# Kernel optimization log

Measured on AMD Instinct MI355X. Metric: run time of the kernel, lower is better.

The kernel has to match this reference:

```python
import jax, jax.numpy as jnp
import numpy as np

EPS = 1e-8  # torch F.cosine_similarity default eps


def setup_inputs() -> dict:
    key = jax.random.key(0)
    k1, k2 = jax.random.split(key)
    x = jax.random.normal(k1, (16384, 1024), dtype=jnp.float32)
    label = jax.random.randint(k2, (16384, 64), 0, 2).astype(jnp.int64)
    w = jnp.asarray(10.0, dtype=jnp.float32)  # nn.Parameter init_w
    b = jnp.asarray(-5.0, dtype=jnp.float32)  # nn.Parameter init_b
    return {"x": x, "label": label, "w": w, "b": b}


def reference(x, label, w, b):
    # Append the 'no-label' column for rows whose label vector is all zero.
    extra = (label.sum(axis=1) == 0).astype(label.dtype)[:, None]
    lab = jnp.concatenate([label, extra], axis=1).astype(x.dtype)  # [B, C]

    counts = lab.sum(axis=0)                  # [C] positives per centroid
    active = counts > 0                       # torch drops empty columns; we mask them

    # Centroids: mean of x over rows carrying each label (scatter-mean as GEMM).
    anchor = (lab.T @ x) / jnp.maximum(counts, 1.0)[:, None]   # [C, D]

    # Cosine similarity between every sample and every centroid.
    xn = jnp.maximum(jnp.linalg.norm(x, axis=1), EPS)          # [B]
    an = jnp.maximum(jnp.linalg.norm(anchor, axis=1), EPS)     # [C]
    cos = (x @ anchor.T) / (xn[:, None] * an[None, :])          # [B, C]

    logits = cos * w + b
    # Removing empty columns from softmax == setting their logits to -inf.
    logits = jnp.where(active[None, :], logits, -jnp.inf)
    logp = jax.nn.log_softmax(logits, axis=1)                   # [B, C]

    # Row expansion in torch duplicates sample i once per positive label j;
    # the logits row only depends on i, so CE over expanded rows is a
    # pair-weighted mean of -logp[i, j] over positive (i, j) pairs.
    n_pairs = lab.sum()
    nloss = -jnp.sum(jnp.where(lab > 0, logp, 0.0)) / n_pairs
    return nloss
```

## Files before the change

### kernel.cpp

```cpp
#include <hip/hip_runtime.h>
#include <hip/hip_bf16.h>
#include <stdint.h>

#define NROWS 16384
#define NDIM  1024
#define NLAB  64
#define NC    65
#define CPAD  80

typedef float float4v __attribute__((ext_vector_type(4)));
typedef short short8  __attribute__((ext_vector_type(8)));

static constexpr size_t SCALE_B = 0;
static constexpr size_t ACTB_B  = 320;
static constexpr size_t WSUM_B  = 400;
static constexpr size_t CNTF_B  = 448;
static constexpr size_t CNTP_B  = 1024;
static constexpr size_t MASK_B  = 83968;
static constexpr size_t XN2_B   = 215040;
static constexpr size_t LFRAG_B = 280576;
static constexpr size_t BFRAG_B = 2902016;
static constexpr size_t XAF_B   = 3065856;
static constexpr size_t PART_B  = 70174720;
static constexpr size_t SLAB    = (size_t)CPAD * NDIM * 4;
static constexpr size_t ANCH_SZ = (size_t)CPAD * NDIM * 4;
static constexpr size_t NRM_SZ  = (size_t)CPAD * 4 * 4;

__device__ __forceinline__ unsigned short bf16u(float f) {
    __hip_bfloat16 h = __float2bfloat16(f);
    return __builtin_bit_cast(unsigned short, h);
}
__device__ __forceinline__ unsigned pk2(float a, float b) {
    return (unsigned)bf16u(a) | ((unsigned)bf16u(b) << 16);
}

__global__ __launch_bounds__(256, 4) void k01_prep(const float* __restrict__ x,
                                                   const int* __restrict__ label,
                                                   unsigned short* __restrict__ xAfrag,
                                                   float* __restrict__ xn2g,
                                                   unsigned long long* __restrict__ masks,
                                                   unsigned* __restrict__ cntpart,
                                                   unsigned short* __restrict__ lfrag) {
    __shared__ unsigned cnt[NC];
    __shared__ unsigned long long smask[64];
    __shared__ float red[4][16];
    int t = threadIdx.x;
    if (blockIdx.x < 1024) {
        int rt = blockIdx.x;
        int w = t >> 6, lane = t & 63, q = lane >> 4, col = lane & 15;
        const float* rowp = x + ((size_t)rt * 16 + col) * NDIM;
        uint4* dst = (uint4*)xAfrag + ((size_t)rt * 32 + w * 8) * 64 + lane;
        float sq = 0.f;
#pragma unroll
        for (int kb = 0; kb < 8; ++kb) {
            int d0 = w * 256 + kb * 32 + q * 8;
            float4 fa = *(const float4*)(rowp + d0);
            float4 fb = *(const float4*)(rowp + d0 + 4);
            sq += fa.x * fa.x + fa.y * fa.y + fa.z * fa.z + fa.w * fa.w
                + fb.x * fb.x + fb.y * fb.y + fb.z * fb.z + fb.w * fb.w;
            uint4 v;
            v.x = pk2(fa.x, fa.y); v.y = pk2(fa.z, fa.w);
            v.z = pk2(fb.x, fb.y); v.w = pk2(fb.z, fb.w);
            dst[kb * 64] = v;
        }
        sq += __shfl_xor(sq, 16, 64);
        sq += __shfl_xor(sq, 32, 64);
        if (q == 0) red[w][col] = sq;
        __syncthreads();
        if (t < 16) xn2g[rt * 16 + t] = red[0][t] + red[1][t] + red[2][t] + red[3][t];
        return;
    }
    int bid = blockIdx.x - 1024;
    if (t < NC) cnt[t] = 0;
    __syncthreads();
    int wave = t >> 6, lane = t & 63;
    int rowblock = bid * 64;
    unsigned creg = 0, zreg = 0;
#pragma unroll 4
    for (int p = 0; p < 16; ++p) {
        int row = rowblock + p * 4 + wave;
        int v = label[row * NLAB + lane];
        unsigned long long m = __ballot(v != 0);
        creg += (unsigned)((m >> lane) & 1ull);
        if (lane == 0) {
            masks[row] = m;
            smask[p * 4 + wave] = m;
            zreg += (m == 0ull) ? 1u : 0u;
        }
    }
    atomicAdd(&cnt[lane], creg);
    if (lane == 0 && zreg) atomicAdd(&cnt[64], zreg);
    __syncthreads();
    if (t < 80) cntpart[bid * 80 + t] = (t < NC) ? cnt[t] : 0u;
    for (int pid = t; pid < 640; pid += 256) {
        int rt2l = pid / 320, rem = pid % 320;
        int ct = rem >> 6, ln = rem & 63;
        int q = ln >> 4, col = ln & 15;
        int c = ct * 16 + col;
        int rbase = rt2l * 32 + q * 8;
        unsigned pk[4];
#pragma unroll
        for (int jp = 0; jp < 4; ++jp) {
            unsigned long long m0 = smask[rbase + jp * 2], m1 = smask[rbase + jp * 2 + 1];
            unsigned b0, b1;
            if (c < 64)       { b0 = (unsigned)((m0 >> c) & 1ull); b1 = (unsigned)((m1 >> c) & 1ull); }
            else if (c == 64) { b0 = (m0 == 0ull); b1 = (m1 == 0ull); }
            else              { b0 = 0u; b1 = 0u; }
            pk[jp] = (b0 ? 0x3F80u : 0u) | (b1 ? 0x3F800000u : 0u);
        }
        uint4 w = make_uint4(pk[0], pk[1], pk[2], pk[3]);
        ((uint4*)lfrag)[((size_t)(bid * 2 + rt2l) * 5 + ct) * 64 + ln] = w;
    }
}

__global__ __launch_bounds__(256) void k2_sums(const float* __restrict__ x,
                                               const unsigned short* __restrict__ lfrag,
                                               float* __restrict__ partial,
                                               int kslices) {
    int t = threadIdx.x, wave = t >> 6, lane = t & 63;
    int q = lane >> 4, col = lane & 15;
    int dgroup = blockIdx.x & 15, ks = blockIdx.x >> 4;
    int nkb = (NROWS / kslices) >> 5;
    int kb0 = ks * nkb;
    int d = dgroup * 64 + wave * 16 + col;
    const uint4* A = (const uint4*)lfrag;
    const float* xb = x + d;

    float4v acc[5];
#pragma unroll
    for (int ct = 0; ct < 5; ++ct) acc[ct] = (float4v){0.f, 0.f, 0.f, 0.f};

    float f0[8], f1[8];
    uint4 a0[5], a1[5];
    {
        const float* p = xb + (size_t)(kb0 * 32 + q * 8) * NDIM;
#pragma unroll
        for (int j = 0; j < 8; ++j) f0[j] = p[(size_t)j * NDIM];
#pragma unroll
        for (int ct = 0; ct < 5; ++ct) a0[ct] = A[((size_t)kb0 * 5 + ct) * 64 + lane];
        const float* p1 = xb + (size_t)((kb0 + 1) * 32 + q * 8) * NDIM;
#pragma unroll
        for (int j = 0; j < 8; ++j) f1[j] = p1[(size_t)j * NDIM];
#pragma unroll
        for (int ct = 0; ct < 5; ++ct) a1[ct] = A[((size_t)(kb0 + 1) * 5 + ct) * 64 + lane];
    }

    for (int i = 0; i < nkb; i += 2) {
        int p2 = i + 2 < nkb ? kb0 + i + 2 : kb0 + i;
        int p3 = i + 3 < nkb ? kb0 + i + 3 : kb0 + i + 1;
        {
            uint4 bq;
            bq.x = pk2(f0[0], f0[1]); bq.y = pk2(f0[2], f0[3]);
            bq.z = pk2(f0[4], f0[5]); bq.w = pk2(f0[6], f0[7]);
            short8 bf = __builtin_bit_cast(short8, bq);
#pragma unroll
            for (int ct = 0; ct < 5; ++ct) {
                short8 af = __builtin_bit_cast(short8, a0[ct]);
                acc[ct] = __builtin_amdgcn_mfma_f32_16x16x32_bf16(af, bf, acc[ct], 0, 0, 0);
            }
            const float* p = xb + (size_t)(p2 * 32 + q * 8) * NDIM;
#pragma unroll
            for (int j = 0; j < 8; ++j) f0[j] = p[(size_t)j * NDIM];
#pragma unroll
            for (int ct = 0; ct < 5; ++ct) a0[ct] = A[((size_t)p2 * 5 + ct) * 64 + lane];
        }
        {
            uint4 bq;
            bq.x = pk2(f1[0], f1[1]); bq.y = pk2(f1[2], f1[3]);
            bq.z = pk2(f1[4], f1[5]); bq.w = pk2(f1[6], f1[7]);
            short8 bf = __builtin_bit_cast(short8, bq);
#pragma unroll
            for (int ct = 0; ct < 5; ++ct) {
                short8 af = __builtin_bit_cast(short8, a1[ct]);
                acc[ct] = __builtin_amdgcn_mfma_f32_16x16x32_bf16(af, bf, acc[ct], 0, 0, 0);
            }
            const float* p = xb + (size_t)(p3 * 32 + q * 8) * NDIM;
#pragma unroll
            for (int j = 0; j < 8; ++j) f1[j] = p[(size_t)j * NDIM];
#pragma unroll
            for (int ct = 0; ct < 5; ++ct) a1[ct] = A[((size_t)p3 * 5 + ct) * 64 + lane];
        }
    }
    float* pb = partial + (size_t)ks * CPAD * NDIM;
#pragma unroll
    for (int ct = 0; ct < 5; ++ct)
#pragma unroll
        for (int reg = 0; reg < 4; ++reg)
            pb[(size_t)(ct * 16 + q * 4 + reg) * NDIM + d] = acc[ct][reg];
}

__global__ __launch_bounds__(256) void k2bA(const float* __restrict__ partial,
                                            int kslices,
                                            float* __restrict__ anchor_raw,
                                            float* __restrict__ norm2part) {
    __shared__ float red[4];
    int c = blockIdx.x >> 2, dq = blockIdx.x & 3, t = threadIdx.x;
    int d = dq * 256 + t;
    const float* p = partial + (size_t)c * NDIM + d;
    float s = 0.f;
#pragma unroll 8
    for (int sl = 0; sl < kslices; ++sl) s += p[(size_t)sl * CPAD * NDIM];
    anchor_raw[(size_t)c * NDIM + d] = s;
    float ss = s * s;
#pragma unroll
    for (int m = 32; m >= 1; m >>= 1) ss += __shfl_xor(ss, m, 64);
    if ((t & 63) == 0) red[t >> 6] = ss;
    __syncthreads();
    if (t == 0) norm2part[blockIdx.x] = red[0] + red[1] + red[2] + red[3];
}

__global__ __launch_bounds__(1024) void k2bB(const float* __restrict__ wptr,
                                             const unsigned* __restrict__ cntpart,
                                             const float* __restrict__ anchor_raw,
                                             const float* __restrict__ norm2part,
                                             unsigned short* __restrict__ bfrag,
                                             float* __restrict__ scale,
                                             unsigned char* __restrict__ actB,
                                             unsigned* __restrict__ countsF,
                                             float* __restrict__ wsum) {
    int c = blockIdx.x, t = threadIdx.x;
    __shared__ float red[16];
    __shared__ unsigned credu[4];
    __shared__ float bcast[1];
    if (c == 0 && t == 512) *wsum = 0.f;
    if (t < 256) {
        unsigned cv = cntpart[t * 80 + c];
#pragma unroll
        for (int m = 32; m >= 1; m >>= 1) cv += __shfl_xor(cv, m, 64);
        if ((t & 63) == 0) credu[t >> 6] = cv;
    }
    if (t == 0)
        bcast[0] = sqrtf(norm2part[c * 4] + norm2part[c * 4 + 1] +
                         norm2part[c * 4 + 2] + norm2part[c * 4 + 3]);
    __syncthreads();
    unsigned cnt = credu[0] + credu[1] + credu[2] + credu[3];
    float invc = 1.0f / (float)(cnt > 0u ? cnt : 1u);
    float a = anchor_raw[(size_t)c * NDIM + t] * invc;
    float an = fmaxf(bcast[0] * invc, 1e-8f);
    unsigned short h = bf16u(a / an);
    int ct = c >> 4, colc = c & 15;
    int kb = t >> 5, q = (t >> 3) & 3, j0 = t & 7;
    bfrag[((((size_t)ct * 32 + kb) * 64) + q * 16 + colc) * 8 + j0] = h;
    float hv = __bfloat162float(__builtin_bit_cast(__hip_bfloat16, h));
    float nb2 = hv * hv;
#pragma unroll
    for (int m = 32; m >= 1; m >>= 1) nb2 += __shfl_xor(nb2, m, 64);
    if ((t & 63) == 0) red[t >> 6] = nb2;
    __syncthreads();
    if (t == 0) {
        float n2 = 0.f;
#pragma unroll
        for (int j = 0; j < 16; ++j) n2 += red[j];
        scale[c] = (n2 > 0.f) ? (wptr[0] / sqrtf(n2)) : 0.f;
        actB[c] = (cnt > 0u) ? 1 : 0;
        countsF[c] = cnt;
    }
}

__global__ __launch_bounds__(256) void k3_loss(const unsigned short* __restrict__ xAfrag,
                                               const unsigned short* __restrict__ bfrag,
                                               const float* __restrict__ xn2g,
                                               const unsigned long long* __restrict__ masks,
                                               const unsigned char* __restrict__ actB,
                                               const float* __restrict__ scale,
                                               const float* __restrict__ bptr,
                                               float* __restrict__ wsum) {
    __shared__ float redsm[3][64][21];
    int t = threadIdx.x, wave = t >> 6, lane = t & 63;
    int q = lane >> 4, col = lane & 15;
    int rt = blockIdx.x;
    int rowbase = rt * 16;
    const uint4* A = (const uint4*)xAfrag + (size_t)rt * 32 * 64 + lane;
    const uint4* Bp = (const uint4*)bfrag + lane;
    int kb0 = wave * 8;

    float4v acc[5];
#pragma unroll
    for (int ct = 0; ct < 5; ++ct) acc[ct] = (float4v){0.f, 0.f, 0.f, 0.f};

    uint4 a0 = A[(size_t)(kb0 + 0) * 64], a1 = A[(size_t)(kb0 + 1) * 64];
    uint4 b0[5], b1[5];
#pragma unroll
    for (int ct = 0; ct < 5; ++ct) b0[ct] = Bp[(size_t)(ct * 32 + kb0 + 0) * 64];
#pragma unroll
    for (int ct = 0; ct < 5; ++ct) b1[ct] = Bp[(size_t)(ct * 32 + kb0 + 1) * 64];

    for (int s = 0; s < 8; s += 2) {
        int p2 = s + 2 < 8 ? kb0 + s + 2 : kb0 + s;
        int p3 = s + 3 < 8 ? kb0 + s + 3 : kb0 + s + 1;
        {
            short8 af = __builtin_bit_cast(short8, a0);
#pragma unroll
            for (int ct = 0; ct < 5; ++ct) {
                short8 bf = __builtin_bit_cast(short8, b0[ct]);
                acc[ct] = __builtin_amdgcn_mfma_f32_16x16x32_bf16(af, bf, acc[ct], 0, 0, 0);
            }
            a0 = A[(size_t)p2 * 64];
#pragma unroll
            for (int ct = 0; ct < 5; ++ct) b0[ct] = Bp[(size_t)(ct * 32 + p2) * 64];
        }
        {
            short8 af = __builtin_bit_cast(short8, a1);
#pragma unroll
            for (int ct = 0; ct < 5; ++ct) {
                short8 bf = __builtin_bit_cast(short8, b1[ct]);
                acc[ct] = __builtin_amdgcn_mfma_f32_16x16x32_bf16(af, bf, acc[ct], 0, 0, 0);
            }
            a1 = A[(size_t)p3 * 64];
#pragma unroll
            for (int ct = 0; ct < 5; ++ct) b1[ct] = Bp[(size_t)(ct * 32 + p3) * 64];
        }
    }

    if (wave) {
#pragma unroll
        for (int ct = 0; ct < 5; ++ct)
#pragma unroll
            for (int reg = 0; reg < 4; ++reg)
                redsm[wave - 1][lane][ct * 4 + reg] = acc[ct][reg];
    }
    __syncthreads();
    if (wave != 0) return;
#pragma unroll
    for (int w = 0; w < 3; ++w)
#pragma unroll
        for (int ct = 0; ct < 5; ++ct)
#pragma unroll
            for (int reg = 0; reg < 4; ++reg)
                acc[ct][reg] += redsm[w][lane][ct * 4 + reg];

    float bv = bptr[0];
    float sc[5]; unsigned char ab[5];
#pragma unroll
    for (int ct = 0; ct < 5; ++ct) { sc[ct] = scale[ct * 16 + col]; ab[ct] = actB[ct * 16 + col]; }

    float contrib = 0.f;
#pragma unroll
    for (int reg = 0; reg < 4; ++reg) {
        int rl = q * 4 + reg;
        int row = rowbase + rl;
        float inv = 1.0f / fmaxf(sqrtf(xn2g[row]), 1e-8f);
        unsigned long long mask = masks[row];
        float v[5]; float lmax = -1e30f;
#pragma unroll
        for (int ct = 0; ct < 5; ++ct) {
            float lg = acc[ct][reg] * sc[ct] * inv + bv;
            v[ct] = ab[ct] ? lg : -1e30f;
            lmax = fmaxf(lmax, v[ct]);
        }
#pragma unroll
        for (int m = 1; m < 16; m <<= 1) lmax = fmaxf(lmax, __shfl_xor(lmax, m, 16));
        float es = 0.f;
#pragma unroll
        for (int ct = 0; ct < 5; ++ct) es += expf(v[ct] - lmax);
#pragma unroll
        for (int m = 1; m < 16; m <<= 1) es += __shfl_xor(es, m, 16);
        float lse = lmax + logf(es);
        float ps = 0.f;
#pragma unroll
        for (int ct = 0; ct < 5; ++ct) {
            int c = ct * 16 + col;
            bool pos = (c < 64) ? (((mask >> c) & 1ull) != 0ull)
                                : ((c == 64) ? (mask == 0ull) : false);
            ps += pos ? v[ct] : 0.f;
        }
#pragma unroll
        for (int m = 1; m < 16; m <<= 1) ps += __shfl_xor(ps, m, 16);
        float npos = mask ? (float)__popcll(mask) : 1.0f;
        float crow = ps - npos * lse;
        if (col == 0) contrib += crow;
    }
#pragma unroll
    for (int m = 1; m < 64; m <<= 1) contrib += __shfl_xor(contrib, m, 64);
    if (lane == 0) atomicAdd(wsum, contrib);
}

__global__ void k4_final(const unsigned* __restrict__ countsF,
                         const float* __restrict__ wsum,
                         float* __restrict__ out) {
    if (threadIdx.x == 0 && blockIdx.x == 0) {
        float np = 0.f;
        for (int c = 0; c < NC; ++c) np += (float)countsF[c];
        out[0] = -wsum[0] / np;
    }
}

extern "C" void kernel_launch(void* const* d_in, const int* in_sizes, int n_in,
                              void* d_out, int out_size, void* d_ws, size_t ws_size,
                              hipStream_t stream) {
    (void)in_sizes; (void)n_in; (void)out_size;
    const float* x = (const float*)d_in[0];
    const int* label = (const int*)d_in[1];
    const float* w = (const float*)d_in[2];
    const float* b = (const float*)d_in[3];

    char* ws = (char*)d_ws;
    float* scale = (float*)(ws + SCALE_B);
    unsigned char* actB = (unsigned char*)(ws + ACTB_B);
    float* wsum = (float*)(ws + WSUM_B);
    unsigned* countsF = (unsigned*)(ws + CNTF_B);
    unsigned* cntpart = (unsigned*)(ws + CNTP_B);
    unsigned long long* masks = (unsigned long long*)(ws + MASK_B);
    float* xn2g = (float*)(ws + XN2_B);
    unsigned short* lfrag = (unsigned short*)(ws + LFRAG_B);
    unsigned short* bfrag = (unsigned short*)(ws + BFRAG_B);
    unsigned short* xAfrag = (unsigned short*)(ws + XAF_B);
    float* partial = (float*)(ws + PART_B);

    int kslices = 64;
    while (kslices > 8 && PART_B + (size_t)kslices * SLAB + ANCH_SZ + NRM_SZ > ws_size)
        kslices >>= 1;
    float* anchor_raw = (float*)(ws + PART_B + (size_t)kslices * SLAB);
    float* norm2part = anchor_raw + CPAD * NDIM;

    hipLaunchKernelGGL(k01_prep, dim3(1024 + 256), dim3(256), 0, stream,
                       x, label, xAfrag, xn2g, masks, cntpart, lfrag);
    hipLaunchKernelGGL(k2_sums, dim3(16 * kslices), dim3(256), 0, stream,
                       x, lfrag, partial, kslices);
    hipLaunchKernelGGL(k2bA, dim3(CPAD * 4), dim3(256), 0, stream,
                       partial, kslices, anchor_raw, norm2part);
    hipLaunchKernelGGL(k2bB, dim3(CPAD), dim3(1024), 0, stream,
                       w, cntpart, anchor_raw, norm2part, bfrag, scale, actB, countsF, wsum);
    hipLaunchKernelGGL(k3_loss, dim3(NROWS / 16), dim3(256), 0, stream,
                       xAfrag, bfrag, xn2g, masks, actB, scale, b, wsum);
    hipLaunchKernelGGL(k4_final, dim3(1), dim3(64), 0, stream, countsF, wsum, (float*)d_out);
}
```

Baseline: 168.5 us.

## Fuse x bf16 conversion and row norms into loss kernel, merge anchor reduction

Drops the prep pass that converted x to bf16 MFMA fragments and computed row norms. The loss kernel now reads fp32 x directly, packs it to bf16 on the fly and accumulates the squared norms itself. The partial-slice reduction for the anchors moves into the centroid-finalize kernel, which removes one launch and the anchor_raw round trip. The default kslices rises to 128. This saves a 32MB bf16 write plus its read-back, but the loss kernel now reads 64MB of fp32 x, and the finalize kernel sums twice as many slices using only 80 blocks.

```diff
diff --git a/kernel.cpp b/kernel.cpp
--- a/kernel.cpp
+++ b/kernel.cpp
@@ -17,14 +17,10 @@
 static constexpr size_t CNTF_B  = 448;
 static constexpr size_t CNTP_B  = 1024;
 static constexpr size_t MASK_B  = 83968;
-static constexpr size_t XN2_B   = 215040;
 static constexpr size_t LFRAG_B = 280576;
 static constexpr size_t BFRAG_B = 2902016;
-static constexpr size_t XAF_B   = 3065856;
-static constexpr size_t PART_B  = 70174720;
+static constexpr size_t PART_B  = 3065856;
 static constexpr size_t SLAB    = (size_t)CPAD * NDIM * 4;
-static constexpr size_t ANCH_SZ = (size_t)CPAD * NDIM * 4;
-static constexpr size_t NRM_SZ  = (size_t)CPAD * 4 * 4;
 
 __device__ __forceinline__ unsigned short bf16u(float f) {
     __hip_bfloat16 h = __float2bfloat16(f);
@@ -34,43 +30,14 @@
     return (unsigned)bf16u(a) | ((unsigned)bf16u(b) << 16);
 }
 
-__global__ __launch_bounds__(256, 4) void k01_prep(const float* __restrict__ x,
-                                                   const int* __restrict__ label,
-                                                   unsigned short* __restrict__ xAfrag,
-                                                   float* __restrict__ xn2g,
-                                                   unsigned long long* __restrict__ masks,
-                                                   unsigned* __restrict__ cntpart,
-                                                   unsigned short* __restrict__ lfrag) {
+__global__ __launch_bounds__(256) void kA_labels(const int* __restrict__ label,
+                                                 unsigned long long* __restrict__ masks,
+                                                 unsigned* __restrict__ cntpart,
+                                                 unsigned short* __restrict__ lfrag) {
     __shared__ unsigned cnt[NC];
     __shared__ unsigned long long smask[64];
-    __shared__ float red[4][16];
     int t = threadIdx.x;
-    if (blockIdx.x < 1024) {
-        int rt = blockIdx.x;
-        int w = t >> 6, lane = t & 63, q = lane >> 4, col = lane & 15;
-        const float* rowp = x + ((size_t)rt * 16 + col) * NDIM;
-        uint4* dst = (uint4*)xAfrag + ((size_t)rt * 32 + w * 8) * 64 + lane;
-        float sq = 0.f;
-#pragma unroll
-        for (int kb = 0; kb < 8; ++kb) {
-            int d0 = w * 256 + kb * 32 + q * 8;
-            float4 fa = *(const float4*)(rowp + d0);
-            float4 fb = *(const float4*)(rowp + d0 + 4);
-            sq += fa.x * fa.x + fa.y * fa.y + fa.z * fa.z + fa.w * fa.w
-                + fb.x * fb.x + fb.y * fb.y + fb.z * fb.z + fb.w * fb.w;
-            uint4 v;
-            v.x = pk2(fa.x, fa.y); v.y = pk2(fa.z, fa.w);
-            v.z = pk2(fb.x, fb.y); v.w = pk2(fb.z, fb.w);
-            dst[kb * 64] = v;
-        }
-        sq += __shfl_xor(sq, 16, 64);
-        sq += __shfl_xor(sq, 32, 64);
-        if (q == 0) red[w][col] = sq;
-        __syncthreads();
-        if (t < 16) xn2g[rt * 16 + t] = red[0][t] + red[1][t] + red[2][t] + red[3][t];
-        return;
-    }
-    int bid = blockIdx.x - 1024;
+    int bid = blockIdx.x;
     if (t < NC) cnt[t] = 0;
     __syncthreads();
     int wave = t >> 6, lane = t & 63;
@@ -113,7 +80,7 @@
     }
 }
 
-__global__ __launch_bounds__(256) void k2_sums(const float* __restrict__ x,
+__global__ __launch_bounds__(256) void kB_sums(const float* __restrict__ x,
                                                const unsigned short* __restrict__ lfrag,
                                                float* __restrict__ partial,
                                                int kslices) {
@@ -189,35 +156,15 @@
             pb[(size_t)(ct * 16 + q * 4 + reg) * NDIM + d] = acc[ct][reg];
 }
 
-__global__ __launch_bounds__(256) void k2bA(const float* __restrict__ partial,
-                                            int kslices,
-                                            float* __restrict__ anchor_raw,
-                                            float* __restrict__ norm2part) {
-    __shared__ float red[4];
-    int c = blockIdx.x >> 2, dq = blockIdx.x & 3, t = threadIdx.x;
-    int d = dq * 256 + t;
-    const float* p = partial + (size_t)c * NDIM + d;
-    float s = 0.f;
-#pragma unroll 8
-    for (int sl = 0; sl < kslices; ++sl) s += p[(size_t)sl * CPAD * NDIM];
-    anchor_raw[(size_t)c * NDIM + d] = s;
-    float ss = s * s;
-#pragma unroll
-    for (int m = 32; m >= 1; m >>= 1) ss += __shfl_xor(ss, m, 64);
-    if ((t & 63) == 0) red[t >> 6] = ss;
-    __syncthreads();
-    if (t == 0) norm2part[blockIdx.x] = red[0] + red[1] + red[2] + red[3];
-}
-
-__global__ __launch_bounds__(1024) void k2bB(const float* __restrict__ wptr,
-                                             const unsigned* __restrict__ cntpart,
-                                             const float* __restrict__ anchor_raw,
-                                             const float* __restrict__ norm2part,
-                                             unsigned short* __restrict__ bfrag,
-                                             float* __restrict__ scale,
-                                             unsigned char* __restrict__ actB,
-                                             unsigned* __restrict__ countsF,
-                                             float* __restrict__ wsum) {
+__global__ __launch_bounds__(1024) void kC_fuse(const float* __restrict__ wptr,
+                                                const unsigned* __restrict__ cntpart,
+                                                const float* __restrict__ partial,
+                                                int kslices,
+                                                unsigned short* __restrict__ bfrag,
+                                                float* __restrict__ scale,
+                                                unsigned char* __restrict__ actB,
+                                                unsigned* __restrict__ countsF,
+                                                float* __restrict__ wsum) {
     int c = blockIdx.x, t = threadIdx.x;
     __shared__ float red[16];
     __shared__ unsigned credu[4];
@@ -229,13 +176,25 @@
         for (int m = 32; m >= 1; m >>= 1) cv += __shfl_xor(cv, m, 64);
         if ((t & 63) == 0) credu[t >> 6] = cv;
     }
-    if (t == 0)
-        bcast[0] = sqrtf(norm2part[c * 4] + norm2part[c * 4 + 1] +
-                         norm2part[c * 4 + 2] + norm2part[c * 4 + 3]);
-    __syncthreads();
+    const float* p = partial + (size_t)c * NDIM + t;
+    float s = 0.f;
+#pragma unroll 8
+    for (int sl = 0; sl < kslices; ++sl) s += p[(size_t)sl * CPAD * NDIM];
+    float ss = s * s;
+#pragma unroll
+    for (int m = 32; m >= 1; m >>= 1) ss += __shfl_xor(ss, m, 64);
+    if ((t & 63) == 0) red[t >> 6] = ss;
+    __syncthreads();
+    if (t == 0) {
+        float tot = 0.f;
+#pragma unroll
+        for (int j = 0; j < 16; ++j) tot += red[j];
+        bcast[0] = sqrtf(tot);
+    }
     unsigned cnt = credu[0] + credu[1] + credu[2] + credu[3];
+    __syncthreads();
     float invc = 1.0f / (float)(cnt > 0u ? cnt : 1u);
-    float a = anchor_raw[(size_t)c * NDIM + t] * invc;
+    float a = s * invc;
     float an = fmaxf(bcast[0] * invc, 1e-8f);
     unsigned short h = bf16u(a / an);
     int ct = c >> 4, colc = c & 15;
@@ -257,61 +216,86 @@
     }
 }
 
-__global__ __launch_bounds__(256) void k3_loss(const unsigned short* __restrict__ xAfrag,
-                                               const unsigned short* __restrict__ bfrag,
-                                               const float* __restrict__ xn2g,
-                                               const unsigned long long* __restrict__ masks,
-                                               const unsigned char* __restrict__ actB,
-                                               const float* __restrict__ scale,
-                                               const float* __restrict__ bptr,
-                                               float* __restrict__ wsum) {
+__global__ __launch_bounds__(256, 4) void kD_loss(const float* __restrict__ x,
+                                                  const unsigned short* __restrict__ bfrag,
+                                                  const unsigned long long* __restrict__ masks,
+                                                  const unsigned char* __restrict__ actB,
+                                                  const float* __restrict__ scale,
+                                                  const float* __restrict__ bptr,
+                                                  float* __restrict__ wsum) {
     __shared__ float redsm[3][64][21];
+    __shared__ float sqred[4][16];
     int t = threadIdx.x, wave = t >> 6, lane = t & 63;
     int q = lane >> 4, col = lane & 15;
     int rt = blockIdx.x;
     int rowbase = rt * 16;
-    const uint4* A = (const uint4*)xAfrag + (size_t)rt * 32 * 64 + lane;
+    const float* rowp = x + ((size_t)rowbase + col) * NDIM;
     const uint4* Bp = (const uint4*)bfrag + lane;
-    int kb0 = wave * 8;
+    int kbg0 = wave * 8;
 
     float4v acc[5];
 #pragma unroll
     for (int ct = 0; ct < 5; ++ct) acc[ct] = (float4v){0.f, 0.f, 0.f, 0.f};
 
-    uint4 a0 = A[(size_t)(kb0 + 0) * 64], a1 = A[(size_t)(kb0 + 1) * 64];
+    float sq = 0.f;
+    float4 fa0, fb0, fa1, fb1;
+    {
+        int d0 = wave * 256 + q * 8;
+        fa0 = *(const float4*)(rowp + d0);
+        fb0 = *(const float4*)(rowp + d0 + 4);
+        fa1 = *(const float4*)(rowp + d0 + 32);
+        fb1 = *(const float4*)(rowp + d0 + 36);
+    }
     uint4 b0[5], b1[5];
 #pragma unroll
-    for (int ct = 0; ct < 5; ++ct) b0[ct] = Bp[(size_t)(ct * 32 + kb0 + 0) * 64];
-#pragma unroll
-    for (int ct = 0; ct < 5; ++ct) b1[ct] = Bp[(size_t)(ct * 32 + kb0 + 1) * 64];
+    for (int ct = 0; ct < 5; ++ct) b0[ct] = Bp[(size_t)(ct * 32 + kbg0 + 0) * 64];
+#pragma unroll
+    for (int ct = 0; ct < 5; ++ct) b1[ct] = Bp[(size_t)(ct * 32 + kbg0 + 1) * 64];
 
     for (int s = 0; s < 8; s += 2) {
-        int p2 = s + 2 < 8 ? kb0 + s + 2 : kb0 + s;
-        int p3 = s + 3 < 8 ? kb0 + s + 3 : kb0 + s + 1;
+        int pl2 = s + 2 < 8 ? s + 2 : s;
+        int pl3 = s + 3 < 8 ? s + 3 : s + 1;
         {
-            short8 af = __builtin_bit_cast(short8, a0);
+            sq += fa0.x * fa0.x + fa0.y * fa0.y + fa0.z * fa0.z + fa0.w * fa0.w
+                + fb0.x * fb0.x + fb0.y * fb0.y + fb0.z * fb0.z + fb0.w * fb0.w;
+            uint4 aq;
+            aq.x = pk2(fa0.x, fa0.y); aq.y = pk2(fa0.z, fa0.w);
+            aq.z = pk2(fb0.x, fb0.y); aq.w = pk2(fb0.z, fb0.w);
+            short8 af = __builtin_bit_cast(short8, aq);
 #pragma unroll
             for (int ct = 0; ct < 5; ++ct) {
                 short8 bf = __builtin_bit_cast(short8, b0[ct]);
                 acc[ct] = __builtin_amdgcn_mfma_f32_16x16x32_bf16(af, bf, acc[ct], 0, 0, 0);
             }
-            a0 = A[(size_t)p2 * 64];
-#pragma unroll
-            for (int ct = 0; ct < 5; ++ct) b0[ct] = Bp[(size_t)(ct * 32 + p2) * 64];
+            int d = wave * 256 + pl2 * 32 + q * 8;
+            fa0 = *(const float4*)(rowp + d);
+            fb0 = *(const float4*)(rowp + d + 4);
+#pragma unroll
+            for (int ct = 0; ct < 5; ++ct) b0[ct] = Bp[(size_t)(ct * 32 + kbg0 + pl2) * 64];
         }
         {
-            short8 af = __builtin_bit_cast(short8, a1);
+            sq += fa1.x * fa1.x + fa1.y * fa1.y + fa1.z * fa1.z + fa1.w * fa1.w
+                + fb1.x * fb1.x + fb1.y * fb1.y + fb1.z * fb1.z + fb1.w * fb1.w;
+            uint4 aq;
+            aq.x = pk2(fa1.x, fa1.y); aq.y = pk2(fa1.z, fa1.w);
+            aq.z = pk2(fb1.x, fb1.y); aq.w = pk2(fb1.z, fb1.w);
+            short8 af = __builtin_bit_cast(short8, aq);
 #pragma unroll
             for (int ct = 0; ct < 5; ++ct) {
                 short8 bf = __builtin_bit_cast(short8, b1[ct]);
                 acc[ct] = __builtin_amdgcn_mfma_f32_16x16x32_bf16(af, bf, acc[ct], 0, 0, 0);
             }
-            a1 = A[(size_t)p3 * 64];
-#pragma unroll
-            for (int ct = 0; ct < 5; ++ct) b1[ct] = Bp[(size_t)(ct * 32 + p3) * 64];
-        }
-    }
-
+            int d = wave * 256 + pl3 * 32 + q * 8;
+            fa1 = *(const float4*)(rowp + d);
+            fb1 = *(const float4*)(rowp + d + 4);
+#pragma unroll
+            for (int ct = 0; ct < 5; ++ct) b1[ct] = Bp[(size_t)(ct * 32 + kbg0 + pl3) * 64];
+        }
+    }
+
+    sq += __shfl_xor(sq, 16, 64);
+    sq += __shfl_xor(sq, 32, 64);
+    if (lane < 16) sqred[wave][lane] = sq;
     if (wave) {
 #pragma unroll
         for (int ct = 0; ct < 5; ++ct)
@@ -339,7 +323,8 @@
     for (int reg = 0; reg < 4; ++reg) {
         int rl = q * 4 + reg;
         int row = rowbase + rl;
-        float inv = 1.0f / fmaxf(sqrtf(xn2g[row]), 1e-8f);
+        float xn2v = sqred[0][rl] + sqred[1][rl] + sqred[2][rl] + sqred[3][rl];
+        float inv = 1.0f / fmaxf(sqrtf(xn2v), 1e-8f);
         unsigned long long mask = masks[row];
         float v[5]; float lmax = -1e30f;
 #pragma unroll
@@ -375,7 +360,7 @@
     if (lane == 0) atomicAdd(wsum, contrib);
 }
 
-__global__ void k4_final(const unsigned* __restrict__ countsF,
+__global__ void kE_final(const unsigned* __restrict__ countsF,
                          const float* __restrict__ wsum,
                          float* __restrict__ out) {
     if (threadIdx.x == 0 && blockIdx.x == 0) {
@@ -401,27 +386,20 @@
     unsigned* countsF = (unsigned*)(ws + CNTF_B);
     unsigned* cntpart = (unsigned*)(ws + CNTP_B);
     unsigned long long* masks = (unsigned long long*)(ws + MASK_B);
-    float* xn2g = (float*)(ws + XN2_B);
     unsigned short* lfrag = (unsigned short*)(ws + LFRAG_B);
     unsigned short* bfrag = (unsigned short*)(ws + BFRAG_B);
-    unsigned short* xAfrag = (unsigned short*)(ws + XAF_B);
     float* partial = (float*)(ws + PART_B);
 
-    int kslices = 64;
-    while (kslices > 8 && PART_B + (size_t)kslices * SLAB + ANCH_SZ + NRM_SZ > ws_size)
-        kslices >>= 1;
-    float* anchor_raw = (float*)(ws + PART_B + (size_t)kslices * SLAB);
-    float* norm2part = anchor_raw + CPAD * NDIM;
-
-    hipLaunchKernelGGL(k01_prep, dim3(1024 + 256), dim3(256), 0, stream,
-                       x, label, xAfrag, xn2g, masks, cntpart, lfrag);
-    hipLaunchKernelGGL(k2_sums, dim3(16 * kslices), dim3(256), 0, stream,
+    int kslices = 128;
+    while (kslices > 8 && PART_B + (size_t)kslices * SLAB > ws_size) kslices >>= 1;
+
+    hipLaunchKernelGGL(kA_labels, dim3(256), dim3(256), 0, stream,
+                       label, masks, cntpart, lfrag);
+    hipLaunchKernelGGL(kB_sums, dim3(16 * kslices), dim3(256), 0, stream,
                        x, lfrag, partial, kslices);
-    hipLaunchKernelGGL(k2bA, dim3(CPAD * 4), dim3(256), 0, stream,
-                       partial, kslices, anchor_raw, norm2part);
-    hipLaunchKernelGGL(k2bB, dim3(CPAD), dim3(1024), 0, stream,
-                       w, cntpart, anchor_raw, norm2part, bfrag, scale, actB, countsF, wsum);
-    hipLaunchKernelGGL(k3_loss, dim3(NROWS / 16), dim3(256), 0, stream,
-                       xAfrag, bfrag, xn2g, masks, actB, scale, b, wsum);
-    hipLaunchKernelGGL(k4_final, dim3(1), dim3(64), 0, stream, countsF, wsum, (float*)d_out);
-}
+    hipLaunchKernelGGL(kC_fuse, dim3(CPAD), dim3(1024), 0, stream,
+                       w, cntpart, partial, kslices, bfrag, scale, actB, countsF, wsum);
+    hipLaunchKernelGGL(kD_loss, dim3(NROWS / 16), dim3(256), 0, stream,
+                       x, bfrag, masks, actB, scale, b, wsum);
+    hipLaunchKernelGGL(kE_final, dim3(1), dim3(64), 0, stream, countsF, wsum, (float*)d_out);
+}
```

Measured after the change: 195.7 us. 1.16x slower.
